# Kernel tuning notes

Measured on AMD Instinct MI355X. Metric: run time of the kernel, lower is better.

## Reference

```python
import jax, jax.numpy as jnp
import numpy as np

# hyperparams (match init_kwargs)
B, T, DV, DJ, L = 32, 256, 1024, 512, 20
K, S, LAYERS = 4, 2, 3
LAM = 4.0            # lambda_softmax used inside frame_by_word attention
MARGIN = 0.1         # opt.global_margin
EPS_BN = 1e-5
EPS_COS = 1e-8


def _bn(x):
    # training-mode BatchNorm1d(affine=False): per-channel stats over (batch, length)
    m = x.mean(axis=(0, 2), keepdims=True)
    v = ((x - m) ** 2).mean(axis=(0, 2), keepdims=True)
    return (x - m) / jnp.sqrt(v + EPS_BN)


def _conv1d(x, w, b, stride):
    # x: [N, Cin, L], w: [Cout, Cin, K], padding=0
    y = jax.lax.conv_general_dilated(x, w, (stride,), 'VALID',
                                     dimension_numbers=('NCH', 'OIH', 'NCH'))
    return y + b[None, :, None]


def setup_inputs() -> dict:
    key = jax.random.key(0)
    ks = jax.random.split(key, 10)
    inp = {
        'video': jax.random.normal(ks[0], (B, T, DV), jnp.float32),
        'words': jax.random.normal(ks[1], (B, L, DJ), jnp.float32),
        'w_masks': jnp.ones((B, L), jnp.float32),
        'conv0_w': jax.random.normal(ks[2], (DJ, DV, K), jnp.float32) * 0.02,
        'conv0_b': jnp.zeros((DJ,), jnp.float32),
        'conv1_w': jax.random.normal(ks[3], (DJ, DJ, K), jnp.float32) * 0.02,
        'conv1_b': jnp.zeros((DJ,), jnp.float32),
        'conv2_w': jax.random.normal(ks[4], (DJ, DJ, K), jnp.float32) * 0.02,
        'conv2_b': jnp.zeros((DJ,), jnp.float32),
        'conv1d_w': jax.random.normal(ks[5], (DJ, DJ, 1), jnp.float32) * 0.02,
        'conv1d_b': jnp.zeros((DJ,), jnp.float32),
    }
    return inp


def reference(video, words, w_masks, conv0_w, conv0_b, conv1_w, conv1_b,
              conv2_w, conv2_b, conv1d_w, conv1d_b):
    # --- conv/batchnorm feature extraction ---
    x = _bn(video.transpose(0, 2, 1))                     # [b, DV, T]
    feats = []
    for w_, b_ in ((conv0_w, conv0_b), (conv1_w, conv1_b), (conv2_w, conv2_b)):
        x = jax.nn.relu(_conv1d(x, w_, b_, S))
        feats.append(x)
    v = jnp.concatenate(feats, axis=-1)                   # [b, DJ, T']
    v = _conv1d(v, conv1d_w, conv1d_b, 1)
    v = _bn(v).transpose(0, 2, 1)                         # [b, T', DJ]
    w = _bn(words.transpose(0, 2, 1)).transpose(0, 2, 1)  # [b, L, DJ]

    # --- batched frame-by-word cross-attention over all (sentence i, video j) pairs ---
    att = jnp.einsum('jtd,ild->ijtl', v, w) * LAM         # [b_i, b_j, T', L]
    mask = (w_masks > 0.5)[:, None, None, :]
    att = jax.nn.softmax(jnp.where(mask, att, -1e9), axis=-1)
    v_s = jnp.einsum('ijtl,ild->ijtd', att, w)            # [b_i, b_j, T', DJ]

    # cosine similarity along feature dim
    num = jnp.einsum('jtd,ijtd->ijt', v, v_s)
    vn = jnp.maximum(jnp.linalg.norm(v, axis=-1), EPS_COS)[None]     # [1, b_j, T']
    vsn = jnp.maximum(jnp.linalg.norm(v_s, axis=-1), EPS_COS)        # [b_i, b_j, T']
    sim = num / (vn * vsn)                                # [b_i, b_j, T']

    b = sim.shape[0]
    idx = jnp.arange(b)
    positive_map = sim[idx, idx]                          # [b, T']
    scores = sim.max(axis=-1)                             # [b_i, b_j]

    # --- diag margin ranking loss ---
    dg = jnp.diagonal(scores)
    cost_s = jnp.clip(MARGIN + scores - dg[:, None], 0.0)
    cost_im = jnp.clip(MARGIN + scores - dg[None, :], 0.0)
    I = jnp.eye(b, dtype=bool)
    cost_s = jnp.where(I, 0.0, cost_s)
    cost_im = jnp.where(I, 0.0, cost_im)
    loss = cost_s.sum() / b + cost_im.sum() / b
    return loss, positive_map
```

## Files before the change

### kernel.cpp

```cpp
#include <hip/hip_runtime.h>
#include <math.h>

#define B_   32
#define T_   256
#define DV_  1024
#define DJ_  512
#define L_   20
#define T0_  127
#define T1_  62
#define T2_  30
#define TP_  219
#define LAM_ 4.0f
#define MARGIN_ 0.1f

typedef __attribute__((ext_vector_type(8))) short short8;
typedef __attribute__((ext_vector_type(4))) float f32x4;

static __device__ __forceinline__ unsigned short f2bf(float f) {
  union { float f; unsigned u; } v; v.f = f;
  unsigned r = v.u + 0x7fff + ((v.u >> 16) & 1);
  return (unsigned short)(r >> 16);
}

struct ushort4_t { unsigned short x, y, z, w; };

#define GLOAD_LDS16(gp, lp)                                                      \
  __builtin_amdgcn_global_load_lds(                                              \
      (const __attribute__((address_space(1))) void*)(gp),                       \
      (__attribute__((address_space(3))) void*)(lp), 16, 0, 0)

__global__ void reorder_all_k(const float* __restrict__ c0w, const float* __restrict__ c1w,
                              const float* __restrict__ c2w, const float* __restrict__ pww,
                              unsigned short* __restrict__ W0, unsigned short* __restrict__ W1,
                              unsigned short* __restrict__ W2, unsigned short* __restrict__ Wp) {
  int bid = blockIdx.x;
  if (bid < 2048) {
    int idx = bid * 256 + threadIdx.x;
    int co = idx >> 10, ci = idx & 1023;
    float4 w = *reinterpret_cast<const float4*>(c0w + (size_t)idx * 4);
    unsigned short* d = W0 + (size_t)co * 4096 + ci;
    d[0] = f2bf(w.x); d[1024] = f2bf(w.y); d[2048] = f2bf(w.z); d[3072] = f2bf(w.w);
  } else if (bid < 3072) {
    int idx = (bid - 2048) * 256 + threadIdx.x;
    int co = idx >> 9, ci = idx & 511;
    float4 w = *reinterpret_cast<const float4*>(c1w + (size_t)idx * 4);
    unsigned short* d = W1 + (size_t)co * 2048 + ci;
    d[0] = f2bf(w.x); d[512] = f2bf(w.y); d[1024] = f2bf(w.z); d[1536] = f2bf(w.w);
  } else if (bid < 4096) {
    int idx = (bid - 3072) * 256 + threadIdx.x;
    int co = idx >> 9, ci = idx & 511;
    float4 w = *reinterpret_cast<const float4*>(c2w + (size_t)idx * 4);
    unsigned short* d = W2 + (size_t)co * 2048 + ci;
    d[0] = f2bf(w.x); d[512] = f2bf(w.y); d[1024] = f2bf(w.z); d[1536] = f2bf(w.w);
  } else {
    int idx = (bid - 4096) * 256 + threadIdx.x;
    float4 v = *reinterpret_cast<const float4*>(pww + (size_t)idx * 4);
    ushort4_t h = { f2bf(v.x), f2bf(v.y), f2bf(v.z), f2bf(v.w) };
    reinterpret_cast<ushort4_t*>(Wp)[idx] = h;
  }
}

__global__ void stats1_k(const float* __restrict__ x, float* __restrict__ part,
                         int C, int rows, int rpg, int cpgShift) {
  int cpg  = 1 << cpgShift;
  int c4   = threadIdx.x & (cpg - 1);
  int rsub = threadIdx.x >> cpgShift;
  int nsub = 256 >> cpgShift;
  int r0 = blockIdx.x * rpg + rsub;
  int r1 = min(blockIdx.x * rpg + rpg, rows);
  float4 s = {0.f,0.f,0.f,0.f}, q = {0.f,0.f,0.f,0.f};
  for (int r = r0; r < r1; r += nsub) {
    float4 v = *reinterpret_cast<const float4*>(&x[(size_t)r * C + c4 * 4]);
    s.x += v.x; s.y += v.y; s.z += v.z; s.w += v.w;
    q.x += v.x*v.x; q.y += v.y*v.y; q.z += v.z*v.z; q.w += v.w*v.w;
  }
  float* ps = part + ((size_t)blockIdx.x * nsub + rsub) * 2 * C;
  reinterpret_cast<float4*>(ps)[c4] = s;
  reinterpret_cast<float4*>(ps + C)[c4] = q;
}

__global__ void stats2_k(const float* __restrict__ part, float* __restrict__ ms,
                         int C, int ng, float inv_n) {
  __shared__ float4 sS[8][33], sQ[8][33];
  int c4l = threadIdx.x & 31;
  int gs  = threadIdx.x >> 5;
  int c4  = blockIdx.x * 32 + c4l;
  float4 s = {0.f,0.f,0.f,0.f}, q = {0.f,0.f,0.f,0.f};
  for (int g = gs; g < ng; g += 8) {
    const float4* ps = reinterpret_cast<const float4*>(part + (size_t)g * 2 * C);
    float4 a = ps[c4];
    float4 b = ps[(C >> 2) + c4];
    s.x += a.x; s.y += a.y; s.z += a.z; s.w += a.w;
    q.x += b.x; q.y += b.y; q.z += b.z; q.w += b.w;
  }
  sS[gs][c4l] = s; sQ[gs][c4l] = q;
  __syncthreads();
  if (gs == 0) {
    float4 S = sS[0][c4l], Q = sQ[0][c4l];
#pragma unroll
    for (int k = 1; k < 8; ++k) {
      float4 a = sS[k][c4l], b = sQ[k][c4l];
      S.x += a.x; S.y += a.y; S.z += a.z; S.w += a.w;
      Q.x += b.x; Q.y += b.y; Q.z += b.z; Q.w += b.w;
    }
    int c = c4 * 4;
    float m0 = S.x * inv_n, m1 = S.y * inv_n, m2 = S.z * inv_n, m3 = S.w * inv_n;
    ms[c+0] = m0; ms[C+c+0] = rsqrtf(Q.x * inv_n - m0*m0 + 1e-5f);
    ms[c+1] = m1; ms[C+c+1] = rsqrtf(Q.y * inv_n - m1*m1 + 1e-5f);
    ms[c+2] = m2; ms[C+c+2] = rsqrtf(Q.z * inv_n - m2*m2 + 1e-5f);
    ms[c+3] = m3; ms[C+c+3] = rsqrtf(Q.w * inv_n - m3*m3 + 1e-5f);
  }
}

__global__ void vid_bn_cast_k(const float* __restrict__ video,
                              const float* __restrict__ ms,
                              unsigned short* __restrict__ vbf) {
  int i4 = blockIdx.x * 256 + threadIdx.x;
  float4 v = reinterpret_cast<const float4*>(video)[i4];
  int c = (i4 & 255) * 4;
  v.x = (v.x - ms[c+0]) * ms[1024+c+0];
  v.y = (v.y - ms[c+1]) * ms[1024+c+1];
  v.z = (v.z - ms[c+2]) * ms[1024+c+2];
  v.w = (v.w - ms[c+3]) * ms[1024+c+3];
  ushort4_t h = { f2bf(v.x), f2bf(v.y), f2bf(v.z), f2bf(v.w) };
  reinterpret_cast<ushort4_t*>(vbf)[i4] = h;
}

template<int BM, int BN, bool RELU, bool BIAS, bool OUT_BF16, bool PARTIAL>
__global__ __launch_bounds__(256) void gemm_k(
    const unsigned short* __restrict__ xin, const unsigned short* __restrict__ Wr,
    const float* __restrict__ bias, void* __restrict__ out,
    int b_stride, int row_off, int row_t_stride,
    int To, int M, int t_off_out, int ldout, int Ktot, int Kloc)
{
  constexpr int AI = BM / 64, BI = BN / 64;
  constexpr int FM = BM / 32, FN = BN / 32;
  __shared__ __align__(16) short As[2][BM * 32];
  __shared__ __align__(16) short Bs[2][BN * 32];

  const int tid  = threadIdx.x;
  const int lane = tid & 63;
  const int wv   = tid >> 6;
  const int wr   = wv >> 1;
  const int wc   = wv & 1;

  const int gx = gridDim.x, gy = gridDim.y;
  const int nwg = gx * gy * gridDim.z;
  const int lin = blockIdx.x + gx * (blockIdx.y + gy * blockIdx.z);
  const int q = nwg >> 3, r = nwg & 7;
  const int xcd = lin & 7, sub = lin >> 3;
  const int work = (xcd < r ? xcd * (q + 1) : r * (q + 1) + (xcd - r) * q) + sub;
  const int bx = work % gx;
  const int by = (work / gx) % gy;
  const int bz = work / (gx * gy);

  const int mbase = bx * BM;
  const int nbase = by * BN;
  const int kstart = PARTIAL ? bz * Kloc : 0;

  const int srow = tid >> 2;
  const int sb   = (((tid & 3) ^ ((srow ^ (srow >> 2)) & 3))) * 8;
  const unsigned short* agp[AI];
  const unsigned short* bgp[BI];
#pragma unroll
  for (int i = 0; i < AI; ++i) {
    int ma = min(mbase + i * 64 + srow, M - 1);
    int b0 = ma / To, t0 = ma % To;
    agp[i] = xin + (size_t)b0 * b_stride + row_off
             + (size_t)t0 * row_t_stride + sb + kstart;
  }
#pragma unroll
  for (int i = 0; i < BI; ++i)
    bgp[i] = Wr + (size_t)(nbase + i * 64 + srow) * Ktot + sb + kstart;

  f32x4 acc[FM][FN] = {};
  const int nsteps = Kloc >> 5;

#define STAGE(buf, k0)                                                \
  do {                                                                \
    _Pragma("unroll")                                                 \
    for (int i = 0; i < AI; ++i)                                      \
      GLOAD_LDS16(agp[i] + (k0), &As[buf][i * 2048 + wv * 512]);      \
    _Pragma("unroll")                                                 \
    for (int i = 0; i < BI; ++i)                                      \
      GLOAD_LDS16(bgp[i] + (k0), &Bs[buf][i * 2048 + wv * 512]);      \
  } while (0)

  STAGE(0, 0);
  __syncthreads();

  const int l15   = lane & 15;
  const int rsw   = (l15 ^ (l15 >> 2)) & 3;
  const int chunk = ((lane >> 4) ^ rsw) * 8;
  const int a_off = (wr * (BM / 2) + l15) * 32 + chunk;
  const int b_off = (wc * (BN / 2) + l15) * 32 + chunk;

  for (int s = 0; s < nsteps; ++s) {
    const int nb = s & 1;
    if (s + 1 < nsteps) STAGE(nb ^ 1, (s + 1) * 32);

    const short* Ab = &As[nb][a_off];
    const short* Bb = &Bs[nb][b_off];
    short8 af[FM], bf[FN];
#pragma unroll
    for (int f = 0; f < FM; ++f)
      af[f] = *reinterpret_cast<const short8*>(Ab + f * 512);
#pragma unroll
    for (int f = 0; f < FN; ++f)
      bf[f] = *reinterpret_cast<const short8*>(Bb + f * 512);
#pragma unroll
    for (int fm = 0; fm < FM; ++fm)
#pragma unroll
      for (int fn = 0; fn < FN; ++fn)
        acc[fm][fn] = __builtin_amdgcn_mfma_f32_16x16x32_bf16(af[fm], bf[fn], acc[fm][fn], 0, 0, 0);

    __syncthreads();
  }
#undef STAGE

  const int cl = lane & 15, rh = lane >> 4;
#pragma unroll
  for (int fm = 0; fm < FM; ++fm) {
#pragma unroll
    for (int fn = 0; fn < FN; ++fn) {
      int col = nbase + wc * (BN / 2) + fn * 16 + cl;
      float bv = BIAS ? bias[col] : 0.f;
      f32x4 v = acc[fm][fn];
#pragma unroll
      for (int rr = 0; rr < 4; ++rr) {
        int m = mbase + wr * (BM / 2) + fm * 16 + rh * 4 + rr;
        if (m < M) {
          if (PARTIAL) {
            float* pout = (float*)out + (size_t)bz * ((size_t)M * ldout);
            pout[(size_t)m * ldout + col] = v[rr];
          } else {
            int b = m / To, to = m % To;
            float x = v[rr] + bv;
            if (RELU) x = fmaxf(x, 0.f);
            size_t oi = ((size_t)b * TP_ + t_off_out + to) * (size_t)ldout + col;
            if (OUT_BF16) ((unsigned short*)out)[oi] = f2bf(x);
            else          ((float*)out)[oi] = x;
          }
        }
      }
    }
  }
}

template<int S>
__global__ void reduce_conv_k(const float* __restrict__ part, const float* __restrict__ bias,
                              unsigned short* __restrict__ outb,
                              int M, int To, int t_off_out) {
  int idx = blockIdx.x * 256 + threadIdx.x;
  int m = idx >> 7, n4 = idx & 127;
  if (m >= M) return;
  size_t off = (size_t)m * 512 + n4 * 4;
  float4 a = *reinterpret_cast<const float4*>(part + off);
#pragma unroll
  for (int s = 1; s < S; ++s) {
    float4 b = *reinterpret_cast<const float4*>(part + (size_t)s * M * 512 + off);
    a.x += b.x; a.y += b.y; a.z += b.z; a.w += b.w;
  }
  float4 bv = *reinterpret_cast<const float4*>(bias + n4 * 4);
  a.x = fmaxf(a.x + bv.x, 0.f);
  a.y = fmaxf(a.y + bv.y, 0.f);
  a.z = fmaxf(a.z + bv.z, 0.f);
  a.w = fmaxf(a.w + bv.w, 0.f);
  int b_ = m / To, to = m % To;
  ushort4_t h = { f2bf(a.x), f2bf(a.y), f2bf(a.z), f2bf(a.w) };
  reinterpret_cast<ushort4_t*>(outb + ((size_t)b_ * TP_ + t_off_out + to) * 512)[n4] = h;
}

__global__ void v2_norm_vn_k(float* __restrict__ v2, const float* __restrict__ ms,
                             unsigned short* __restrict__ v2bf, float* __restrict__ vn) {
  int r = blockIdx.x, t = threadIdx.x;
  float* row = v2 + (size_t)r * DJ_;
  unsigned short* brow = v2bf + (size_t)r * DJ_;
  float ss = 0.f;
#pragma unroll
  for (int h = 0; h < 2; ++h) {
    int c4 = t + h * 64;
    float4 v = reinterpret_cast<float4*>(row)[c4];
    int c = c4 * 4;
    v.x = (v.x - ms[c+0]) * ms[DJ_+c+0];
    v.y = (v.y - ms[c+1]) * ms[DJ_+c+1];
    v.z = (v.z - ms[c+2]) * ms[DJ_+c+2];
    v.w = (v.w - ms[c+3]) * ms[DJ_+c+3];
    reinterpret_cast<float4*>(row)[c4] = v;
    ushort4_t h4 = { f2bf(v.x), f2bf(v.y), f2bf(v.z), f2bf(v.w) };
    reinterpret_cast<ushort4_t*>(brow)[c4] = h4;
    ss += v.x*v.x + v.y*v.y + v.z*v.z + v.w*v.w;
  }
#pragma unroll
  for (int o = 32; o; o >>= 1) ss += __shfl_down(ss, o, 64);
  if (t == 0) vn[r] = sqrtf(ss);
}

__global__ void wnorm_k(const float* __restrict__ words, const float* __restrict__ ms,
                        float* __restrict__ wbn, unsigned short* __restrict__ wbnb) {
  int idx = blockIdx.x * 256 + threadIdx.x;
  if (idx >= (B_ * L_ * DJ_) / 4) return;
  int c = (idx & 127) * 4;
  float4 v = reinterpret_cast<const float4*>(words)[idx];
  v.x = (v.x - ms[c+0]) * ms[DJ_+c+0];
  v.y = (v.y - ms[c+1]) * ms[DJ_+c+1];
  v.z = (v.z - ms[c+2]) * ms[DJ_+c+2];
  v.w = (v.w - ms[c+3]) * ms[DJ_+c+3];
  reinterpret_cast<float4*>(wbn)[idx] = v;
  ushort4_t h = { f2bf(v.x), f2bf(v.y), f2bf(v.z), f2bf(v.w) };
  reinterpret_cast<ushort4_t*>(wbnb)[idx] = h;
}

__global__ void gram_k(const float* __restrict__ wbn, float* __restrict__ G) {
  __shared__ float sw[L_ * 516];
  int i = blockIdx.x, tid = threadIdx.x;
  for (int idx = tid; idx < L_ * DJ_; idx += 256) {
    int l = idx >> 9, d = idx & 511;
    sw[l * 516 + d] = wbn[(size_t)i * L_ * DJ_ + idx];
  }
  __syncthreads();
  for (int p = tid; p < L_ * L_; p += 256) {
    int l = p / L_, l2 = p % L_;
    const float4* a = reinterpret_cast<const float4*>(&sw[l * 516]);
    const float4* b = reinterpret_cast<const float4*>(&sw[l2 * 516]);
    float acc = 0.f;
    for (int d4 = 0; d4 < 128; ++d4) {
      float4 av = a[d4], bv = b[d4];
      acc += av.x*bv.x + av.y*bv.y + av.z*bv.z + av.w*bv.w;
    }
    G[i * 400 + p] = acc;
  }
}

__global__ __launch_bounds__(256) void sim_k(
    const float* __restrict__ A, const float* __restrict__ G,
    const float* __restrict__ vn, const float* __restrict__ wmask,
    float* __restrict__ pos, float* __restrict__ scores) {
  int j = blockIdx.x, i = blockIdx.y;
  __shared__ float sG[400];
  __shared__ float sm[20];
  __shared__ float red[4];
  int tid = threadIdx.x;
  for (int p = tid; p < 400; p += 256) sG[p] = G[i * 400 + p];
  if (tid < 20) sm[tid] = wmask[i * 20 + tid];
  __syncthreads();

  float simv = -1e30f;
  if (tid < TP_) {
    const float* ar = A + ((size_t)j * TP_ + tid) * 640 + i * 20;
    float a[20], p[20];
    float mx = -1e30f;
#pragma unroll
    for (int l = 0; l < 20; ++l) {
      a[l] = ar[l];
      float lg = (sm[l] > 0.5f) ? LAM_ * a[l] : -1e9f;
      p[l] = lg;
      mx = fmaxf(mx, lg);
    }
    float Z = 0.f;
#pragma unroll
    for (int l = 0; l < 20; ++l) { p[l] = __expf(p[l] - mx); Z += p[l]; }
    float invZ = 1.f / Z, num = 0.f;
#pragma unroll
    for (int l = 0; l < 20; ++l) { p[l] *= invZ; num += p[l] * a[l]; }
    float q2 = 0.f;
#pragma unroll
    for (int l = 0; l < 20; ++l) {
      float gi = 0.f;
#pragma unroll
      for (int l2 = 0; l2 < 20; ++l2) gi += sG[l * 20 + l2] * p[l2];
      q2 += p[l] * gi;
    }
    float vnv = fmaxf(vn[(size_t)j * TP_ + tid], 1e-8f);
    float vsnv = fmaxf(sqrtf(q2), 1e-8f);
    simv = num / (vnv * vsnv);
    if (i == j) pos[i * TP_ + tid] = simv;
  }
  float mv = simv;
#pragma unroll
  for (int o = 32; o; o >>= 1) mv = fmaxf(mv, __shfl_down(mv, o, 64));
  if ((tid & 63) == 0) red[tid >> 6] = mv;
  __syncthreads();
  if (tid == 0)
    scores[i * 32 + j] = fmaxf(fmaxf(red[0], red[1]), fmaxf(red[2], red[3]));
}

__global__ void loss_k(const float* __restrict__ scores, float* __restrict__ out) {
  __shared__ float red[16];
  int tid = threadIdx.x;
  int i = tid >> 5, j = tid & 31;
  float s = scores[tid];
  float dgi = scores[i * 32 + i], dgj = scores[j * 32 + j];
  float c = 0.f;
  if (i != j)
    c = fmaxf(0.f, MARGIN_ + s - dgi) + fmaxf(0.f, MARGIN_ + s - dgj);
#pragma unroll
  for (int o = 32; o; o >>= 1) c += __shfl_down(c, o, 64);
  if ((tid & 63) == 0) red[tid >> 6] = c;
  __syncthreads();
  if (tid == 0) {
    float t = 0.f;
    for (int w = 0; w < 16; ++w) t += red[w];
    out[0] = t / 32.f;
  }
}

extern "C" void kernel_launch(void* const* d_in, const int* in_sizes, int n_in,
                              void* d_out, int out_size, void* d_ws, size_t ws_size,
                              hipStream_t stream) {
  const float* video = (const float*)d_in[0];
  const float* words = (const float*)d_in[1];
  const float* wmask = (const float*)d_in[2];
  const float* c0w = (const float*)d_in[3];
  const float* c0b = (const float*)d_in[4];
  const float* c1w = (const float*)d_in[5];
  const float* c1b = (const float*)d_in[6];
  const float* c2w = (const float*)d_in[7];
  const float* c2b = (const float*)d_in[8];
  const float* pww = (const float*)d_in[9];
  const float* pwb = (const float*)d_in[10];
  float* out = (float*)d_out;
  float* ws  = (float*)d_ws;

  float*          W0r    = ws;
  float*          W1r    = W0r + 1048576;
  float*          W2r    = W1r + 524288;
  float*          Wpw    = W2r + 524288;
  float*          AMvbf  = Wpw + 131072;
  float*          vcatb  = AMvbf + 4485120;
  float*          Pbuf   = vcatb + 1794048;
  float*          v2     = Pbuf;
  float*          v2bfp  = v2 + 3588096;
  float*          wbn    = v2bfp + 1794048;
  float*          wbnbp  = wbn + 327680;
  float*          G      = wbnbp + 163840;
  float*          vn     = G + 12800;
  float*          scores = vn + 7008;
  float*          vpart  = scores + 1024;
  float*          vms    = vpart + 1048576;
  float*          v2part = vms + 2048;
  float*          v2ms   = v2part + 897024;
  float*          wpart  = v2ms + 1024;
  float*          wms    = wpart + 81920;

  unsigned short* W0     = (unsigned short*)W0r;
  unsigned short* W1     = (unsigned short*)W1r;
  unsigned short* W2     = (unsigned short*)W2r;
  unsigned short* Wp     = (unsigned short*)Wpw;
  unsigned short* vbf    = (unsigned short*)AMvbf;
  float*          Amat   = AMvbf;
  unsigned short* vcb    = (unsigned short*)vcatb;
  unsigned short* v2bf   = (unsigned short*)v2bfp;
  unsigned short* wbnb   = (unsigned short*)wbnbp;

  reorder_all_k<<<4352, 256, 0, stream>>>(c0w, c1w, c2w, pww, W0, W1, W2, Wp);

  stats1_k<<<512, 256, 0, stream>>>(video, vpart, 1024, 8192, 16, 8);
  stats2_k<<<8, 256, 0, stream>>>(vpart, vms, 1024, 512, 1.f / 8192.f);
  vid_bn_cast_k<<<8192, 256, 0, stream>>>(video, vms, vbf);

  gemm_k<64, 128, false, false, false, true><<<dim3(64, 4, 4), 256, 0, stream>>>(
      vbf, W0, nullptr, Pbuf, 262144, 0, 2048, T0_, 32 * T0_, 0, 512, 4096, 1024);
  reduce_conv_k<4><<<2032, 256, 0, stream>>>(Pbuf, c0b, vcb, 32 * T0_, T0_, 0);
  gemm_k<64, 128, false, false, false, true><<<dim3(31, 4, 8), 256, 0, stream>>>(
      vcb, W1, nullptr, Pbuf, 112128, 0, 1024, T1_, 32 * T1_, 0, 512, 2048, 256);
  reduce_conv_k<8><<<992, 256, 0, stream>>>(Pbuf, c1b, vcb, 32 * T1_, T1_, T0_);
  gemm_k<64, 64, false, false, false, true><<<dim3(15, 8, 8), 256, 0, stream>>>(
      vcb, W2, nullptr, Pbuf, 112128, 65024, 1024, T2_, 32 * T2_, 0, 512, 2048, 256);
  reduce_conv_k<8><<<480, 256, 0, stream>>>(Pbuf, c2b, vcb, 32 * T2_, T2_, T0_ + T1_);

  gemm_k<64, 64, false, true, false, false><<<dim3(110, 8), 256, 0, stream>>>(
      vcb, Wp, pwb, v2, 112128, 0, 512, TP_, 32 * TP_, 0, 512, 512, 512);

  stats1_k<<<438, 256, 0, stream>>>(v2, v2part, 512, 7008, 16, 7);
  stats2_k<<<4, 256, 0, stream>>>(v2part, v2ms, 512, 876, 1.f / 7008.f);
  v2_norm_vn_k<<<7008, 64, 0, stream>>>(v2, v2ms, v2bf, vn);

  stats1_k<<<40, 256, 0, stream>>>(words, wpart, 512, 640, 16, 7);
  stats2_k<<<4, 256, 0, stream>>>(wpart, wms, 512, 80, 1.f / 640.f);
  wnorm_k<<<(81920 + 255) / 256, 256, 0, stream>>>(words, wms, wbn, wbnb);
  gram_k<<<32, 256, 0, stream>>>(wbn, G);

  gemm_k<64, 64, false, false, false, false><<<dim3(110, 10), 256, 0, stream>>>(
      v2bf, wbnb, nullptr, Amat, 112128, 0, 512, TP_, 32 * TP_, 0, 640, 512, 512);

  sim_k<<<dim3(32, 32), 256, 0, stream>>>(Amat, G, vn, wmask, out + 1, scores);
  loss_k<<<1, 1024, 0, stream>>>(scores, out);
}
```

Baseline: 244.3 us.

## Merge prep kernels and fuse pointwise-conv BN stats into GEMM epilogue

Weight reordering, video and word stats passes are merged into one launch, the two stats reductions into one, and the video cast plus word normalization and Gram computation into another. The pointwise conv GEMM now accumulates per-channel sum and sum of squares in its epilogue, which removes a separate full read of v2. This cuts the launch count and memory traffic but adds a shared-memory reduction and a sync to the GEMM epilogue, and changes the workspace layout.

```diff
diff --git a/kernel.cpp b/kernel.cpp
--- a/kernel.cpp
+++ b/kernel.cpp
@@ -29,62 +29,35 @@
       (const __attribute__((address_space(1))) void*)(gp),                       \
       (__attribute__((address_space(3))) void*)(lp), 16, 0, 0)
 
-__global__ void reorder_all_k(const float* __restrict__ c0w, const float* __restrict__ c1w,
-                              const float* __restrict__ c2w, const float* __restrict__ pww,
-                              unsigned short* __restrict__ W0, unsigned short* __restrict__ W1,
-                              unsigned short* __restrict__ W2, unsigned short* __restrict__ Wp) {
-  int bid = blockIdx.x;
-  if (bid < 2048) {
-    int idx = bid * 256 + threadIdx.x;
-    int co = idx >> 10, ci = idx & 1023;
-    float4 w = *reinterpret_cast<const float4*>(c0w + (size_t)idx * 4);
-    unsigned short* d = W0 + (size_t)co * 4096 + ci;
-    d[0] = f2bf(w.x); d[1024] = f2bf(w.y); d[2048] = f2bf(w.z); d[3072] = f2bf(w.w);
-  } else if (bid < 3072) {
-    int idx = (bid - 2048) * 256 + threadIdx.x;
-    int co = idx >> 9, ci = idx & 511;
-    float4 w = *reinterpret_cast<const float4*>(c1w + (size_t)idx * 4);
-    unsigned short* d = W1 + (size_t)co * 2048 + ci;
-    d[0] = f2bf(w.x); d[512] = f2bf(w.y); d[1024] = f2bf(w.z); d[1536] = f2bf(w.w);
-  } else if (bid < 4096) {
-    int idx = (bid - 3072) * 256 + threadIdx.x;
-    int co = idx >> 9, ci = idx & 511;
-    float4 w = *reinterpret_cast<const float4*>(c2w + (size_t)idx * 4);
-    unsigned short* d = W2 + (size_t)co * 2048 + ci;
-    d[0] = f2bf(w.x); d[512] = f2bf(w.y); d[1024] = f2bf(w.z); d[1536] = f2bf(w.w);
-  } else {
-    int idx = (bid - 4096) * 256 + threadIdx.x;
-    float4 v = *reinterpret_cast<const float4*>(pww + (size_t)idx * 4);
-    ushort4_t h = { f2bf(v.x), f2bf(v.y), f2bf(v.z), f2bf(v.w) };
-    reinterpret_cast<ushort4_t*>(Wp)[idx] = h;
-  }
-}
-
-__global__ void stats1_k(const float* __restrict__ x, float* __restrict__ part,
-                         int C, int rows, int rpg, int cpgShift) {
+__device__ __forceinline__ void stats1_body(const float* __restrict__ x,
+                                            float* __restrict__ part,
+                                            int C, int rows, int rpg, int cpgShift,
+                                            int bid, int tid) {
   int cpg  = 1 << cpgShift;
-  int c4   = threadIdx.x & (cpg - 1);
-  int rsub = threadIdx.x >> cpgShift;
+  int c4   = tid & (cpg - 1);
+  int rsub = tid >> cpgShift;
   int nsub = 256 >> cpgShift;
-  int r0 = blockIdx.x * rpg + rsub;
-  int r1 = min(blockIdx.x * rpg + rpg, rows);
+  int r0 = bid * rpg + rsub;
+  int r1 = min(bid * rpg + rpg, rows);
   float4 s = {0.f,0.f,0.f,0.f}, q = {0.f,0.f,0.f,0.f};
   for (int r = r0; r < r1; r += nsub) {
     float4 v = *reinterpret_cast<const float4*>(&x[(size_t)r * C + c4 * 4]);
     s.x += v.x; s.y += v.y; s.z += v.z; s.w += v.w;
     q.x += v.x*v.x; q.y += v.y*v.y; q.z += v.z*v.z; q.w += v.w*v.w;
   }
-  float* ps = part + ((size_t)blockIdx.x * nsub + rsub) * 2 * C;
+  float* ps = part + ((size_t)bid * nsub + rsub) * 2 * C;
   reinterpret_cast<float4*>(ps)[c4] = s;
   reinterpret_cast<float4*>(ps + C)[c4] = q;
 }
 
-__global__ void stats2_k(const float* __restrict__ part, float* __restrict__ ms,
-                         int C, int ng, float inv_n) {
-  __shared__ float4 sS[8][33], sQ[8][33];
-  int c4l = threadIdx.x & 31;
-  int gs  = threadIdx.x >> 5;
-  int c4  = blockIdx.x * 32 + c4l;
+__device__ __forceinline__ void stats2_body(const float* __restrict__ part,
+                                            float* __restrict__ ms,
+                                            int C, int ng, float inv_n,
+                                            int bid, int tid,
+                                            float4* sS, float4* sQ) {
+  int c4l = tid & 31;
+  int gs  = tid >> 5;
+  int c4  = bid * 32 + c4l;
   float4 s = {0.f,0.f,0.f,0.f}, q = {0.f,0.f,0.f,0.f};
   for (int g = gs; g < ng; g += 8) {
     const float4* ps = reinterpret_cast<const float4*>(part + (size_t)g * 2 * C);
@@ -93,13 +66,13 @@
     s.x += a.x; s.y += a.y; s.z += a.z; s.w += a.w;
     q.x += b.x; q.y += b.y; q.z += b.z; q.w += b.w;
   }
-  sS[gs][c4l] = s; sQ[gs][c4l] = q;
+  sS[gs * 33 + c4l] = s; sQ[gs * 33 + c4l] = q;
   __syncthreads();
   if (gs == 0) {
-    float4 S = sS[0][c4l], Q = sQ[0][c4l];
+    float4 S = sS[c4l], Q = sQ[c4l];
 #pragma unroll
     for (int k = 1; k < 8; ++k) {
-      float4 a = sS[k][c4l], b = sQ[k][c4l];
+      float4 a = sS[k * 33 + c4l], b = sQ[k * 33 + c4l];
       S.x += a.x; S.y += a.y; S.z += a.z; S.w += a.w;
       Q.x += b.x; Q.y += b.y; Q.z += b.z; Q.w += b.w;
     }
@@ -112,24 +85,100 @@
   }
 }
 
-__global__ void vid_bn_cast_k(const float* __restrict__ video,
-                              const float* __restrict__ ms,
-                              unsigned short* __restrict__ vbf) {
-  int i4 = blockIdx.x * 256 + threadIdx.x;
-  float4 v = reinterpret_cast<const float4*>(video)[i4];
-  int c = (i4 & 255) * 4;
-  v.x = (v.x - ms[c+0]) * ms[1024+c+0];
-  v.y = (v.y - ms[c+1]) * ms[1024+c+1];
-  v.z = (v.z - ms[c+2]) * ms[1024+c+2];
-  v.w = (v.w - ms[c+3]) * ms[1024+c+3];
-  ushort4_t h = { f2bf(v.x), f2bf(v.y), f2bf(v.z), f2bf(v.w) };
-  reinterpret_cast<ushort4_t*>(vbf)[i4] = h;
-}
-
-template<int BM, int BN, bool RELU, bool BIAS, bool OUT_BF16, bool PARTIAL>
+__global__ void prep_k(const float* __restrict__ c0w, const float* __restrict__ c1w,
+                       const float* __restrict__ c2w, const float* __restrict__ pww,
+                       unsigned short* __restrict__ W0, unsigned short* __restrict__ W1,
+                       unsigned short* __restrict__ W2, unsigned short* __restrict__ Wp,
+                       const float* __restrict__ video, float* __restrict__ vpart,
+                       const float* __restrict__ words, float* __restrict__ wpart) {
+  int bid = blockIdx.x, tid = threadIdx.x;
+  if (bid < 2048) {
+    int idx = bid * 256 + tid;
+    int co = idx >> 10, ci = idx & 1023;
+    float4 w = *reinterpret_cast<const float4*>(c0w + (size_t)idx * 4);
+    unsigned short* d = W0 + (size_t)co * 4096 + ci;
+    d[0] = f2bf(w.x); d[1024] = f2bf(w.y); d[2048] = f2bf(w.z); d[3072] = f2bf(w.w);
+  } else if (bid < 3072) {
+    int idx = (bid - 2048) * 256 + tid;
+    int co = idx >> 9, ci = idx & 511;
+    float4 w = *reinterpret_cast<const float4*>(c1w + (size_t)idx * 4);
+    unsigned short* d = W1 + (size_t)co * 2048 + ci;
+    d[0] = f2bf(w.x); d[512] = f2bf(w.y); d[1024] = f2bf(w.z); d[1536] = f2bf(w.w);
+  } else if (bid < 4096) {
+    int idx = (bid - 3072) * 256 + tid;
+    int co = idx >> 9, ci = idx & 511;
+    float4 w = *reinterpret_cast<const float4*>(c2w + (size_t)idx * 4);
+    unsigned short* d = W2 + (size_t)co * 2048 + ci;
+    d[0] = f2bf(w.x); d[512] = f2bf(w.y); d[1024] = f2bf(w.z); d[1536] = f2bf(w.w);
+  } else if (bid < 4352) {
+    int idx = (bid - 4096) * 256 + tid;
+    float4 v = *reinterpret_cast<const float4*>(pww + (size_t)idx * 4);
+    ushort4_t h = { f2bf(v.x), f2bf(v.y), f2bf(v.z), f2bf(v.w) };
+    reinterpret_cast<ushort4_t*>(Wp)[idx] = h;
+  } else if (bid < 4864) {
+    stats1_body(video, vpart, 1024, 8192, 16, 8, bid - 4352, tid);
+  } else {
+    stats1_body(words, wpart, 512, 640, 16, 7, bid - 4864, tid);
+  }
+}
+
+__global__ void stats2c_k(const float* __restrict__ vpart, float* __restrict__ vms,
+                          const float* __restrict__ wpart, float* __restrict__ wms) {
+  __shared__ float4 sS[8 * 33], sQ[8 * 33];
+  int bid = blockIdx.x, tid = threadIdx.x;
+  if (bid < 8) stats2_body(vpart, vms, 1024, 512, 1.f / 8192.f, bid, tid, sS, sQ);
+  else         stats2_body(wpart, wms, 512,  80,  1.f / 640.f,  bid - 8, tid, sS, sQ);
+}
+
+__global__ void stats2_k(const float* __restrict__ part, float* __restrict__ ms,
+                         int C, int ng, float inv_n) {
+  __shared__ float4 sS[8 * 33], sQ[8 * 33];
+  stats2_body(part, ms, C, ng, inv_n, blockIdx.x, threadIdx.x, sS, sQ);
+}
+
+__global__ void cast_wgram_k(const float* __restrict__ video, const float* __restrict__ vms,
+                             unsigned short* __restrict__ vbf,
+                             const float* __restrict__ words, const float* __restrict__ wms,
+                             unsigned short* __restrict__ wbnb, float* __restrict__ G) {
+  __shared__ float sw[L_ * 516];
+  int bid = blockIdx.x, tid = threadIdx.x;
+  if (bid < 8192) {
+    int i4 = bid * 256 + tid;
+    float4 v = reinterpret_cast<const float4*>(video)[i4];
+    int c = (i4 & 255) * 4;
+    v.x = (v.x - vms[c+0]) * vms[1024+c+0];
+    v.y = (v.y - vms[c+1]) * vms[1024+c+1];
+    v.z = (v.z - vms[c+2]) * vms[1024+c+2];
+    v.w = (v.w - vms[c+3]) * vms[1024+c+3];
+    ushort4_t h = { f2bf(v.x), f2bf(v.y), f2bf(v.z), f2bf(v.w) };
+    reinterpret_cast<ushort4_t*>(vbf)[i4] = h;
+  } else {
+    int i = bid - 8192;
+    for (int idx = tid; idx < L_ * DJ_; idx += 256) {
+      int l = idx >> 9, d = idx & 511;
+      float x = (words[(size_t)i * L_ * DJ_ + idx] - wms[d]) * wms[DJ_ + d];
+      sw[l * 516 + d] = x;
+      wbnb[(size_t)i * L_ * DJ_ + idx] = f2bf(x);
+    }
+    __syncthreads();
+    for (int p = tid; p < L_ * L_; p += 256) {
+      int l = p / L_, l2 = p % L_;
+      const float4* a = reinterpret_cast<const float4*>(&sw[l * 516]);
+      const float4* b = reinterpret_cast<const float4*>(&sw[l2 * 516]);
+      float acc = 0.f;
+      for (int d4 = 0; d4 < 128; ++d4) {
+        float4 av = a[d4], bv = b[d4];
+        acc += av.x*bv.x + av.y*bv.y + av.z*bv.z + av.w*bv.w;
+      }
+      G[i * 400 + p] = acc;
+    }
+  }
+}
+
+template<int BM, int BN, bool RELU, bool BIAS, bool OUT_BF16, bool PARTIAL, bool STATS>
 __global__ __launch_bounds__(256) void gemm_k(
     const unsigned short* __restrict__ xin, const unsigned short* __restrict__ Wr,
-    const float* __restrict__ bias, void* __restrict__ out,
+    const float* __restrict__ bias, void* __restrict__ out, float* __restrict__ spart,
     int b_stride, int row_off, int row_t_stride,
     int To, int M, int t_off_out, int ldout, int Ktot, int Kloc)
 {
@@ -137,6 +186,7 @@
   constexpr int FM = BM / 32, FN = BN / 32;
   __shared__ __align__(16) short As[2][BM * 32];
   __shared__ __align__(16) short Bs[2][BN * 32];
+  __shared__ float wred[4][2][32];
 
   const int tid  = threadIdx.x;
   const int lane = tid & 63;
@@ -219,6 +269,9 @@
 #undef STAGE
 
   const int cl = lane & 15, rh = lane >> 4;
+  float ls[FN], lq[FN];
+#pragma unroll
+  for (int f = 0; f < FN; ++f) { ls[f] = 0.f; lq[f] = 0.f; }
 #pragma unroll
   for (int fm = 0; fm < FM; ++fm) {
 #pragma unroll
@@ -240,9 +293,29 @@
             size_t oi = ((size_t)b * TP_ + t_off_out + to) * (size_t)ldout + col;
             if (OUT_BF16) ((unsigned short*)out)[oi] = f2bf(x);
             else          ((float*)out)[oi] = x;
+            if (STATS) { ls[fn] += x; lq[fn] += x * x; }
           }
         }
       }
+    }
+  }
+
+  if (STATS) {
+#pragma unroll
+    for (int fn = 0; fn < FN; ++fn) {
+      float s = ls[fn], qq = lq[fn];
+      s  += __shfl_xor(s, 16, 64);  qq += __shfl_xor(qq, 16, 64);
+      s  += __shfl_xor(s, 32, 64);  qq += __shfl_xor(qq, 32, 64);
+      if (rh == 0) { wred[wv][0][fn * 16 + cl] = s; wred[wv][1][fn * 16 + cl] = qq; }
+    }
+    __syncthreads();
+    if (tid < 64) {
+      int wc2 = tid >> 5, cl2 = tid & 31;
+      float s  = wred[wc2][0][cl2] + wred[wc2 + 2][0][cl2];
+      float qq = wred[wc2][1][cl2] + wred[wc2 + 2][1][cl2];
+      int chan = nbase + wc2 * 32 + cl2;
+      spart[(size_t)bx * 1024 + chan]       = s;
+      spart[(size_t)bx * 1024 + 512 + chan] = qq;
     }
   }
 }
@@ -294,42 +367,6 @@
 #pragma unroll
   for (int o = 32; o; o >>= 1) ss += __shfl_down(ss, o, 64);
   if (t == 0) vn[r] = sqrtf(ss);
-}
-
-__global__ void wnorm_k(const float* __restrict__ words, const float* __restrict__ ms,
-                        float* __restrict__ wbn, unsigned short* __restrict__ wbnb) {
-  int idx = blockIdx.x * 256 + threadIdx.x;
-  if (idx >= (B_ * L_ * DJ_) / 4) return;
-  int c = (idx & 127) * 4;
-  float4 v = reinterpret_cast<const float4*>(words)[idx];
-  v.x = (v.x - ms[c+0]) * ms[DJ_+c+0];
-  v.y = (v.y - ms[c+1]) * ms[DJ_+c+1];
-  v.z = (v.z - ms[c+2]) * ms[DJ_+c+2];
-  v.w = (v.w - ms[c+3]) * ms[DJ_+c+3];
-  reinterpret_cast<float4*>(wbn)[idx] = v;
-  ushort4_t h = { f2bf(v.x), f2bf(v.y), f2bf(v.z), f2bf(v.w) };
-  reinterpret_cast<ushort4_t*>(wbnb)[idx] = h;
-}
-
-__global__ void gram_k(const float* __restrict__ wbn, float* __restrict__ G) {
-  __shared__ float sw[L_ * 516];
-  int i = blockIdx.x, tid = threadIdx.x;
-  for (int idx = tid; idx < L_ * DJ_; idx += 256) {
-    int l = idx >> 9, d = idx & 511;
-    sw[l * 516 + d] = wbn[(size_t)i * L_ * DJ_ + idx];
-  }
-  __syncthreads();
-  for (int p = tid; p < L_ * L_; p += 256) {
-    int l = p / L_, l2 = p % L_;
-    const float4* a = reinterpret_cast<const float4*>(&sw[l * 516]);
-    const float4* b = reinterpret_cast<const float4*>(&sw[l2 * 516]);
-    float acc = 0.f;
-    for (int d4 = 0; d4 < 128; ++d4) {
-      float4 av = a[d4], bv = b[d4];
-      acc += av.x*bv.x + av.y*bv.y + av.z*bv.z + av.w*bv.w;
-    }
-    G[i * 400 + p] = acc;
-  }
 }
 
 __global__ __launch_bounds__(256) void sim_k(
@@ -431,17 +468,17 @@
   float*          Pbuf   = vcatb + 1794048;
   float*          v2     = Pbuf;
   float*          v2bfp  = v2 + 3588096;
-  float*          wbn    = v2bfp + 1794048;
-  float*          wbnbp  = wbn + 327680;
+  float*          v2part = v2bfp + 1794048;
+  float*          v2ms   = v2part + 112640;
+  float*          vpart  = v2ms + 1024;
+  float*          vms    = vpart + 1048576;
+  float*          wpart  = vms + 2048;
+  float*          wms    = wpart + 81920;
+  float*          endPb  = Pbuf + 8323072;
+  float*          wbnbp  = endPb;
   float*          G      = wbnbp + 163840;
   float*          vn     = G + 12800;
   float*          scores = vn + 7008;
-  float*          vpart  = scores + 1024;
-  float*          vms    = vpart + 1048576;
-  float*          v2part = vms + 2048;
-  float*          v2ms   = v2part + 897024;
-  float*          wpart  = v2ms + 1024;
-  float*          wms    = wpart + 81920;
 
   unsigned short* W0     = (unsigned short*)W0r;
   unsigned short* W1     = (unsigned short*)W1r;
@@ -453,36 +490,29 @@
   unsigned short* v2bf   = (unsigned short*)v2bfp;
   unsigned short* wbnb   = (unsigned short*)wbnbp;
 
-  reorder_all_k<<<4352, 256, 0, stream>>>(c0w, c1w, c2w, pww, W0, W1, W2, Wp);
-
-  stats1_k<<<512, 256, 0, stream>>>(video, vpart, 1024, 8192, 16, 8);
-  stats2_k<<<8, 256, 0, stream>>>(vpart, vms, 1024, 512, 1.f / 8192.f);
-  vid_bn_cast_k<<<8192, 256, 0, stream>>>(video, vms, vbf);
-
-  gemm_k<64, 128, false, false, false, true><<<dim3(64, 4, 4), 256, 0, stream>>>(
-      vbf, W0, nullptr, Pbuf, 262144, 0, 2048, T0_, 32 * T0_, 0, 512, 4096, 1024);
+  prep_k<<<4904, 256, 0, stream>>>(c0w, c1w, c2w, pww, W0, W1, W2, Wp,
+                                   video, vpart, words, wpart);
+  stats2c_k<<<12, 256, 0, stream>>>(vpart, vms, wpart, wms);
+  cast_wgram_k<<<8224, 256, 0, stream>>>(video, vms, vbf, words, wms, wbnb, G);
+
+  gemm_k<64, 128, false, false, false, true, false><<<dim3(64, 4, 4), 256, 0, stream>>>(
+      vbf, W0, nullptr, Pbuf, nullptr, 262144, 0, 2048, T0_, 32 * T0_, 0, 512, 4096, 1024);
   reduce_conv_k<4><<<2032, 256, 0, stream>>>(Pbuf, c0b, vcb, 32 * T0_, T0_, 0);
-  gemm_k<64, 128, false, false, false, true><<<dim3(31, 4, 8), 256, 0, stream>>>(
-      vcb, W1, nullptr, Pbuf, 112128, 0, 1024, T1_, 32 * T1_, 0, 512, 2048, 256);
+  gemm_k<64, 128, false, false, false, true, false><<<dim3(31, 4, 8), 256, 0, stream>>>(
+      vcb, W1, nullptr, Pbuf, nullptr, 112128, 0, 1024, T1_, 32 * T1_, 0, 512, 2048, 256);
   reduce_conv_k<8><<<992, 256, 0, stream>>>(Pbuf, c1b, vcb, 32 * T1_, T1_, T0_);
-  gemm_k<64, 64, false, false, false, true><<<dim3(15, 8, 8), 256, 0, stream>>>(
-      vcb, W2, nullptr, Pbuf, 112128, 65024, 1024, T2_, 32 * T2_, 0, 512, 2048, 256);
+  gemm_k<64, 64, false, false, false, true, false><<<dim3(15, 8, 8), 256, 0, stream>>>(
+      vcb, W2, nullptr, Pbuf, nullptr, 112128, 65024, 1024, T2_, 32 * T2_, 0, 512, 2048, 256);
   reduce_conv_k<8><<<480, 256, 0, stream>>>(Pbuf, c2b, vcb, 32 * T2_, T2_, T0_ + T1_);
 
-  gemm_k<64, 64, false, true, false, false><<<dim3(110, 8), 256, 0, stream>>>(
-      vcb, Wp, pwb, v2, 112128, 0, 512, TP_, 32 * TP_, 0, 512, 512, 512);
-
-  stats1_k<<<438, 256, 0, stream>>>(v2, v2part, 512, 7008, 16, 7);
-  stats2_k<<<4, 256, 0, stream>>>(v2part, v2ms, 512, 876, 1.f / 7008.f);
+  gemm_k<64, 64, false, true, false, false, true><<<dim3(110, 8), 256, 0, stream>>>(
+      vcb, Wp, pwb, v2, v2part, 112128, 0, 512, TP_, 32 * TP_, 0, 512, 512, 512);
+
+  stats2_k<<<4, 256, 0, stream>>>(v2part, v2ms, 512, 110, 1.f / 7008.f);
   v2_norm_vn_k<<<7008, 64, 0, stream>>>(v2, v2ms, v2bf, vn);
 
-  stats1_k<<<40, 256, 0, stream>>>(words, wpart, 512, 640, 16, 7);
-  stats2_k<<<4, 256, 0, stream>>>(wpart, wms, 512, 80, 1.f / 640.f);
-  wnorm_k<<<(81920 + 255) / 256, 256, 0, stream>>>(words, wms, wbn, wbnb);
-  gram_k<<<32, 256, 0, stream>>>(wbn, G);
-
-  gemm_k<64, 64, false, false, false, false><<<dim3(110, 10), 256, 0, stream>>>(
-      v2bf, wbnb, nullptr, Amat, 112128, 0, 512, TP_, 32 * TP_, 0, 640, 512, 512);
+  gemm_k<64, 64, false, false, false, false, false><<<dim3(110, 10), 256, 0, stream>>>(
+      v2bf, wbnb, nullptr, Amat, nullptr, 112128, 0, 512, TP_, 32 * TP_, 0, 640, 512, 512);
 
   sim_k<<<dim3(32, 32), 256, 0, stream>>>(Amat, G, vn, wmask, out + 1, scores);
   loss_k<<<1, 1024, 0, stream>>>(scores, out);
```

Result: faster. 206.0 us (-15.7%).
